# Performance work log

Measured on AMD Instinct MI355X. Metric: run time of the kernel, lower is better.

Reference implementation:

```python
import jax, jax.numpy as jnp
import numpy as np

K = 499  # kernel_size


def setup_inputs() -> dict:
    key = jax.random.key(0)
    k1, k2 = jax.random.split(key)
    B, F, T = 32, 64, 8000
    # nonnegative spectrogram input, shape (B, 1, F, T)
    x = jax.random.uniform(k1, (B, 1, F, T), dtype=jnp.float32)
    a = 0.90 + 0.099 * jax.random.uniform(k2, (F,), dtype=jnp.float32)
    w = jnp.ones((F,), dtype=jnp.float32)
    return {"x": x, "a": a, "w": w}


def _build_kernel(a, w, dtype):
    # powers[f, k] = a_f ** k, k = 0..K-2
    F = a.shape[0]
    powers = a[:, None] ** jnp.arange(K - 1, dtype=dtype)  # (F, K-1)
    C = 1.0 / powers.sum(axis=1)                            # (F,)
    neg = (-C * w)[:, None] * powers                        # (F, K-1)
    # pre-flip kernel = [1, neg_0, ..., neg_{K-2}]; flipped -> [neg_{K-2}, ..., neg_0, 1]
    kern = jnp.concatenate([neg[:, ::-1], jnp.ones((F, 1), dtype)], axis=1)  # (F, K)
    return kern[:, None, :]  # (F, 1, K) OIH, groups = F


def reference(x, a, w):
    dtype = x.dtype
    kern = _build_kernel(a.astype(dtype), w.astype(dtype), dtype)
    xs = x[:, 0]  # (B, F, T)
    # replicate (edge) pad on the left by K-1 along time
    xp = jnp.pad(xs, ((0, 0), (0, 0), (K - 1, 0)), mode="edge")
    y = jax.lax.conv_general_dilated(
        xp, kern,
        window_strides=(1,), padding="VALID",
        dimension_numbers=("NCH", "OIH", "NCH"),
        feature_group_count=xs.shape[1],
    )  # (B, F, T)
    return jnp.abs(y)[:, None]  # (B, 1, F, T)
```

## Files before the change

kernel.cpp:

```cpp
#include <hip/hip_runtime.h>
#include <math.h>


constexpr int T     = 8000;
constexpr int F     = 64;
constexpr int B     = 32;
constexpr int KM1   = 498;
constexpr int CHUNK = 512;
constexpr int CPR   = 16;

#define DPP_F(x, ctrl, rm) \
  __builtin_bit_cast(float, __builtin_amdgcn_update_dpp(0, __builtin_bit_cast(int, (x)), (ctrl), (rm), 0xf, false))

__device__ __forceinline__ double dpow(double b, int e) {
    double r = 1.0, p = b;
    while (e) { if (e & 1) r *= p; p *= p; e >>= 1; }
    return r;
}

__device__ __forceinline__ float powi(float base, int e) {
    float r = 1.0f, p = base;
    #pragma unroll
    for (int b = 0; b < 9; ++b) { r = (e & (1 << b)) ? r * p : r; p *= p; }
    return r;
}

__device__ __forceinline__ int swz(int i) { return i ^ (((i >> 5) & 7) << 2); }

__global__ __launch_bounds__(1024, 1) void willmore_scan_kernel(
    const float* __restrict__ x, const float* __restrict__ a,
    const float* __restrict__ w, float* __restrict__ out)
{
    __shared__ float lx[CPR * CHUNK];

    const int chunk = threadIdx.x >> 6;
    const int lane  = threadIdx.x & 63;
    const int row   = blockIdx.x;
    const int f     = row & (F - 1);

    const float* xr   = x   + (size_t)row * T;
    float*       orow = out + (size_t)row * T;

    const int t0   = chunk * CHUNK;
    const int tb_u = t0 + 8 * lane;
    const int tb   = min(tb_u, T - 8);

    const float4 m0 = *(const float4*)(xr + tb);
    const float4 m1 = *(const float4*)(xr + tb + 4);

    const double ad     = (double)a[f];
    const double a498d  = dpow(ad, KM1);
    const double sumgeo = (1.0 - a498d) / (1.0 - ad);
    const double r_d    = dpow(ad, 8);
    const float  af     = (float)ad;
    const float  na498  = (float)(-a498d);
    const float  g      = (float)(1.0 / sumgeo) * w[f];
    const float  r1     = (float)r_d;
    const float  r2     = (float)(r_d * r_d);
    const float  r4     = (float)dpow(r_d, 4);
    const float  r8     = (float)dpow(r_d, 8);
    const float  inv_r  = (float)(1.0 / r_d);
    const float  alane  = powi(af, 8 * lane);
    const float  wA     = powi(af, 8 * ((lane & 15) + 1));
    const float  wB     = powi(af, 8 * ((lane & 31) + 1));

    *(float4*)(&lx[swz(tb)])     = m0;
    *(float4*)(&lx[swz(tb + 4)]) = m1;
    __syncthreads();

    float S;
    if (chunk == 0) {
        S = lx[0] * (float)sumgeo;
    } else {
        const int wb = t0 - CHUNK + 8 * lane;
        const float4 w0 = *(const float4*)(&lx[swz(wb)]);
        const float4 w1 = *(const float4*)(&lx[swz(wb + 4)]);
        float ws8[8] = {w0.x, w0.y, w0.z, w0.w, w1.x, w1.y, w1.z, w1.w};
        #pragma unroll
        for (int i = 0; i < 8; ++i) { if (8 * lane + i < 14) ws8[i] = 0.0f; }
        float h = ws8[0];
        #pragma unroll
        for (int i = 1; i < 8; ++i) h = fmaf(h, af, ws8[i]);
        float contrib = powi(af, 504 - 8 * lane) * h;
        #pragma unroll
        for (int s = 1; s < 64; s <<= 1) contrib += __shfl_xor(contrib, s, 64);
        S = contrib;
    }

    const int lg = tb - KM1;
    float lv[8];
    if (chunk == 0) {
        #pragma unroll
        for (int i = 0; i < 8; ++i) lv[i] = lx[swz(max(lg + i, 0))];
    } else {
        #pragma unroll
        for (int i = 0; i < 4; ++i) {
            const float2 p = *(const float2*)(&lx[swz(lg + 2 * i)]);
            lv[2 * i]     = p.x;
            lv[2 * i + 1] = p.y;
        }
    }

    const float xv[8] = {m0.x, m0.y, m0.z, m0.w, m1.x, m1.y, m1.z, m1.w};
    float u[8];
    #pragma unroll
    for (int i = 0; i < 8; ++i) u[i] = fmaf(na498, lv[i], xv[i]);

    float q = u[0];
    #pragma unroll
    for (int i = 1; i < 8; ++i) q = fmaf(q, af, u[i]);

    float G = q;
    G = fmaf(r1, DPP_F(G, 0x111, 0xf), G);
    G = fmaf(r2, DPP_F(G, 0x112, 0xf), G);
    G = fmaf(r4, DPP_F(G, 0x114, 0xf), G);
    G = fmaf(r8, DPP_F(G, 0x118, 0xf), G);
    G = fmaf(wA, DPP_F(G, 0x142, 0xa), G);
    G = fmaf(wB, DPP_F(G, 0x143, 0xc), G);

    const float E = (G - q) * inv_r;

    float s = fmaf(alane, S, E);
    float y[8];
    #pragma unroll
    for (int i = 0; i < 8; ++i) {
        y[i] = fabsf(fmaf(-g, s, xv[i]));
        s = fmaf(af, s, u[i]);
    }

    if (tb_u <= T - 8) {
        *(float4*)(orow + tb)     = make_float4(y[0], y[1], y[2], y[3]);
        *(float4*)(orow + tb + 4) = make_float4(y[4], y[5], y[6], y[7]);
    }
}

extern "C" void kernel_launch(void* const* d_in, const int* in_sizes, int n_in,
                              void* d_out, int out_size, void* d_ws, size_t ws_size,
                              hipStream_t stream) {
    const float* x = (const float*)d_in[0];
    const float* a = (const float*)d_in[1];
    const float* w = (const float*)d_in[2];
    float* out = (float*)d_out;

    hipLaunchKernelGGL(willmore_scan_kernel, dim3(B * F), dim3(1024), 0, stream,
                       x, a, w, out);
}
```

Before: 115.0 us.

## Split each row across two 512-thread blocks and compute constants once per block

Each row is now split across two 512-thread blocks, one per half of the time axis, instead of one 1024-thread block. The second half also loads one halo chunk of the preceding samples into shared memory so it can compute its carry-in window sum. The double-precision per-band constants are now computed by a single thread and broadcast through shared memory, rather than recomputed by every thread. This is meant to raise occupancy and cut redundant FP64 work. In exchange it adds a redundant halo load and an extra read through shared memory.

```diff
diff --git a/kernel.cpp b/kernel.cpp
--- a/kernel.cpp
+++ b/kernel.cpp
@@ -7,7 +7,8 @@
 constexpr int B     = 32;
 constexpr int KM1   = 498;
 constexpr int CHUNK = 512;
-constexpr int CPR   = 16;
+constexpr int HALF  = 4096;
+constexpr int LXN   = HALF + CHUNK;
 
 #define DPP_F(x, ctrl, rm) \
   __builtin_bit_cast(float, __builtin_amdgcn_update_dpp(0, __builtin_bit_cast(int, (x)), (ctrl), (rm), 0xf, false))
@@ -27,54 +28,71 @@
 
 __device__ __forceinline__ int swz(int i) { return i ^ (((i >> 5) & 7) << 2); }
 
-__global__ __launch_bounds__(1024, 1) void willmore_scan_kernel(
+__global__ __launch_bounds__(512, 4) void willmore_scan_kernel(
     const float* __restrict__ x, const float* __restrict__ a,
     const float* __restrict__ w, float* __restrict__ out)
 {
-    __shared__ float lx[CPR * CHUNK];
+    __shared__ float lx[LXN];
+    __shared__ float cb[8];
 
-    const int chunk = threadIdx.x >> 6;
-    const int lane  = threadIdx.x & 63;
-    const int row   = blockIdx.x;
-    const int f     = row & (F - 1);
+    const int tid  = threadIdx.x;
+    const int cl   = tid >> 6;
+    const int lane = tid & 63;
+    const int row  = blockIdx.x >> 1;
+    const int half = blockIdx.x & 1;
+    const int f    = row & (F - 1);
+    const int h0   = half * HALF;
 
     const float* xr   = x   + (size_t)row * T;
     float*       orow = out + (size_t)row * T;
 
-    const int t0   = chunk * CHUNK;
+    const int t0   = h0 + cl * CHUNK;
     const int tb_u = t0 + 8 * lane;
     const int tb   = min(tb_u, T - 8);
+    const int lb   = tb - h0 + CHUNK;
 
     const float4 m0 = *(const float4*)(xr + tb);
     const float4 m1 = *(const float4*)(xr + tb + 4);
+    float4 hv;
+    if (half && tid < 128)
+        hv = *(const float4*)(xr + h0 - CHUNK + 4 * tid);
 
-    const double ad     = (double)a[f];
-    const double a498d  = dpow(ad, KM1);
-    const double sumgeo = (1.0 - a498d) / (1.0 - ad);
-    const double r_d    = dpow(ad, 8);
-    const float  af     = (float)ad;
-    const float  na498  = (float)(-a498d);
-    const float  g      = (float)(1.0 / sumgeo) * w[f];
-    const float  r1     = (float)r_d;
-    const float  r2     = (float)(r_d * r_d);
-    const float  r4     = (float)dpow(r_d, 4);
-    const float  r8     = (float)dpow(r_d, 8);
-    const float  inv_r  = (float)(1.0 / r_d);
-    const float  alane  = powi(af, 8 * lane);
-    const float  wA     = powi(af, 8 * ((lane & 15) + 1));
-    const float  wB     = powi(af, 8 * ((lane & 31) + 1));
+    const float af    = a[f];
+    const float alane = powi(af, 8 * lane);
+    const float wA    = powi(af, 8 * ((lane & 15) + 1));
+    const float wB    = powi(af, 8 * ((lane & 31) + 1));
 
-    *(float4*)(&lx[swz(tb)])     = m0;
-    *(float4*)(&lx[swz(tb + 4)]) = m1;
+    if (tid == 0) {
+        const double ad     = (double)af;
+        const double a498d  = dpow(ad, KM1);
+        const double sumgeo = (1.0 - a498d) / (1.0 - ad);
+        const double r_d    = dpow(ad, 8);
+        cb[0] = (float)(-a498d);
+        cb[1] = (float)(1.0 / sumgeo) * w[f];
+        cb[2] = (float)r_d;
+        cb[3] = (float)(r_d * r_d);
+        cb[4] = (float)dpow(r_d, 4);
+        cb[5] = (float)dpow(r_d, 8);
+        cb[6] = (float)(1.0 / r_d);
+        cb[7] = (float)sumgeo;
+    }
+
+    *(float4*)(&lx[swz(lb)])     = m0;
+    *(float4*)(&lx[swz(lb + 4)]) = m1;
+    if (half && tid < 128)
+        *(float4*)(&lx[swz(4 * tid)]) = hv;
     __syncthreads();
 
+    const float na498 = cb[0], g  = cb[1], r1    = cb[2], r2 = cb[3],
+                r4    = cb[4], r8 = cb[5], inv_r = cb[6];
+
     float S;
-    if (chunk == 0) {
-        S = lx[0] * (float)sumgeo;
+    if (half == 0 && cl == 0) {
+        S = lx[swz(CHUNK)] * cb[7];
     } else {
-        const int wb = t0 - CHUNK + 8 * lane;
-        const float4 w0 = *(const float4*)(&lx[swz(wb)]);
-        const float4 w1 = *(const float4*)(&lx[swz(wb + 4)]);
+        const int wl = cl * CHUNK + 8 * lane;
+        const float4 w0 = *(const float4*)(&lx[swz(wl)]);
+        const float4 w1 = *(const float4*)(&lx[swz(wl + 4)]);
         float ws8[8] = {w0.x, w0.y, w0.z, w0.w, w1.x, w1.y, w1.z, w1.w};
         #pragma unroll
         for (int i = 0; i < 8; ++i) { if (8 * lane + i < 14) ws8[i] = 0.0f; }
@@ -89,13 +107,14 @@
 
     const int lg = tb - KM1;
     float lv[8];
-    if (chunk == 0) {
+    if (half == 0 && cl == 0) {
         #pragma unroll
-        for (int i = 0; i < 8; ++i) lv[i] = lx[swz(max(lg + i, 0))];
+        for (int i = 0; i < 8; ++i) lv[i] = lx[swz(max(lg + i, 0) + CHUNK)];
     } else {
+        const int ll = lg - h0 + CHUNK;
         #pragma unroll
         for (int i = 0; i < 4; ++i) {
-            const float2 p = *(const float2*)(&lx[swz(lg + 2 * i)]);
+            const float2 p = *(const float2*)(&lx[swz(ll + 2 * i)]);
             lv[2 * i]     = p.x;
             lv[2 * i + 1] = p.y;
         }
@@ -142,6 +161,6 @@
     const float* w = (const float*)d_in[2];
     float* out = (float*)d_out;
 
-    hipLaunchKernelGGL(willmore_scan_kernel, dim3(B * F), dim3(1024), 0, stream,
+    hipLaunchKernelGGL(willmore_scan_kernel, dim3(B * F * 2), dim3(512), 0, stream,
                        x, a, w, out);
 }
```

Result: no change. 113.2 us (-1.6%).
